# Performance work log

Hardware: AMD Instinct MI355X
Metric: run time of the kernel (lower is better)

## Reference

```python
import jax, jax.numpy as jnp
import numpy as np

B, C, N = 4, 256, 4096
BN_EPS = 1e-5


def setup_inputs() -> dict:
    key = jax.random.key(0)
    ks = jax.random.split(key, 8)
    Cq = C // 4
    return {
        "x": jax.random.normal(ks[0], (B, C, N), dtype=jnp.float32),
        # q_conv and k_conv share weights (self.q_conv.weight = self.k_conv.weight)
        "w_qk": jax.random.normal(ks[1], (Cq, C), dtype=jnp.float32) * 0.05,
        "w_v": jax.random.normal(ks[2], (C, C), dtype=jnp.float32) * 0.05,
        "b_v": jax.random.normal(ks[3], (C,), dtype=jnp.float32) * 0.05,
        # LBR: Conv1d(C,C,1) + BN1d (inference stats) + ReLU
        "w_lbr": jax.random.normal(ks[4], (C, C), dtype=jnp.float32) * 0.05,
        "b_lbr": jax.random.normal(ks[5], (C,), dtype=jnp.float32) * 0.05,
        "bn_gamma": jnp.ones((C,), dtype=jnp.float32),
        "bn_beta": jnp.zeros((C,), dtype=jnp.float32),
        "bn_mean": jax.random.normal(ks[6], (C,), dtype=jnp.float32) * 0.05,
        "bn_var": jax.random.uniform(ks[7], (C,), dtype=jnp.float32, minval=0.5, maxval=1.5),
    }


def reference(x, w_qk, w_v, b_v, w_lbr, b_lbr, bn_gamma, bn_beta, bn_mean, bn_var):
    # x: [B, C, N]
    chans = x.shape[1]
    # conv1x1 Q/K (shared weight, no bias), V (with bias)
    x_q = jnp.einsum('qc,bcn->bnq', w_qk, x)          # [B, N, C/4]
    x_k = jnp.einsum('qc,bcm->bqm', w_qk, x)          # [B, C/4, N]
    x_v = jnp.einsum('oc,bcn->bon', w_v, x) + b_v[None, :, None]  # [B, C, N]
    # energy: [B, N_query, N_key]
    energy = jnp.einsum('bnq,bqm->bnm', x_q, x_k)
    # 'SL' normalization: scale by C**-0.5, softmax over dim=-2 (query axis)
    energy = energy * (chans ** -0.5)
    attention = jax.nn.softmax(energy, axis=-2)        # [B, N, N]
    # x_r[b,c,m] = sum_n x_v[b,c,n] * attention[b,n,m]
    x_r = jnp.einsum('bcn,bnm->bcm', x_v, attention)   # [B, C, N]
    # offset residual
    x_r = x - x_r
    # LBR: conv1x1 -> BN (inference) -> ReLU
    h = jnp.einsum('oc,bcn->bon', w_lbr, x_r) + b_lbr[None, :, None]
    inv_std = jax.lax.rsqrt(bn_var + BN_EPS)
    h = (h - bn_mean[None, :, None]) * (inv_std * bn_gamma)[None, :, None] + bn_beta[None, :, None]
    h = jax.nn.relu(h)
    return x + h
```

## Files before the change

kernel.cpp:

```cpp
#include <hip/hip_runtime.h>
#include <hip/hip_bf16.h>
#include <stdint.h>
#include <math.h>

#define Bq 4
#define Cc 256
#define Nn 4096
#define CQ 64
#define QKSCALE 0.30028060219661246f

typedef short s16x4 __attribute__((ext_vector_type(4)));
typedef short s16x8 __attribute__((ext_vector_type(8)));
typedef unsigned int u32x4 __attribute__((ext_vector_type(4)));
typedef float f32x16 __attribute__((ext_vector_type(16)));

#define MFMA32(a,b,c) __builtin_amdgcn_mfma_f32_32x32x16_bf16((a),(b),(c),0,0,0)

static __device__ __forceinline__ unsigned short f2b(float f) {
  unsigned int u = __float_as_uint(f);
  u += 0x7FFFu + ((u >> 16) & 1u);
  return (unsigned short)(u >> 16);
}

static __device__ __forceinline__ unsigned short f2bh(float f) {
  __hip_bfloat16 h = __float2bfloat16(f);
  return __builtin_bit_cast(unsigned short, h);
}

static __device__ __forceinline__ float b2f(unsigned short u) {
  return __uint_as_float(((unsigned int)u) << 16);
}

static __device__ __forceinline__ float fexp2(float x) {
#if __has_builtin(__builtin_amdgcn_exp2f)
  return __builtin_amdgcn_exp2f(x);
#else
  return exp2f(x);
#endif
}

static __device__ __forceinline__ f32x16 fz16() {
  f32x16 z;
#pragma unroll
  for (int i = 0; i < 16; i++) z[i] = 0.0f;
  return z;
}

static __device__ __forceinline__ float sum16(f32x16 E) {
  return (((E[0] + E[1]) + (E[2] + E[3])) + ((E[4] + E[5]) + (E[6] + E[7]))) +
         (((E[8] + E[9]) + (E[10] + E[11])) + ((E[12] + E[13]) + (E[14] + E[15])));
}

__global__ __launch_bounds__(256) void k_prep(
    const float* __restrict__ wqk, const float* __restrict__ wv,
    const float* __restrict__ wlbr, const float* __restrict__ blbr,
    const float* __restrict__ gamma, const float* __restrict__ beta,
    const float* __restrict__ mean, const float* __restrict__ var,
    unsigned short* __restrict__ Wcat, float* __restrict__ sd) {
  int bx = blockIdx.x, t = threadIdx.x;
  if (bx < 576) {
    float v;
    if (bx < 64) v = wqk[bx * 256 + t] * QKSCALE;
    else if (bx < 320) v = wv[(bx - 64) * 256 + t];
    else v = wlbr[(bx - 320) * 256 + t];
    Wcat[bx * 256 + t] = f2b(v);
  } else {
    float s = gamma[t] * rsqrtf(var[t] + 1e-5f);
    sd[t] = s;
    sd[256 + t] = beta[t] + (blbr[t] - mean[t]) * s;
  }
}

__global__ __launch_bounds__(640) void k_proj(const float* __restrict__ x,
                                              const unsigned short* __restrict__ Wcat,
                                              const float* __restrict__ bv,
                                              unsigned short* __restrict__ qkT,
                                              unsigned short* __restrict__ Vf,
                                              unsigned short* __restrict__ xT) {
  __shared__ unsigned short xs[32 * 264];
  int bx = blockIdx.x;
  int b = bx >> 7;
  int ntile = bx & 127;
  int n0 = ntile * 32;
  int t = threadIdx.x;
  const float* xb = x + (size_t)b * Cc * Nn;
  for (int u = t; u < 1024; u += 640) {
    int c = u >> 2, j = (u & 3) * 8;
    const float* src = &xb[(size_t)c * Nn + n0 + j];
    float4 v0 = *(const float4*)src;
    float4 v1 = *(const float4*)(src + 4);
    xs[(j + 0) * 264 + c] = f2b(v0.x);
    xs[(j + 1) * 264 + c] = f2b(v0.y);
    xs[(j + 2) * 264 + c] = f2b(v0.z);
    xs[(j + 3) * 264 + c] = f2b(v0.w);
    xs[(j + 4) * 264 + c] = f2b(v1.x);
    xs[(j + 5) * 264 + c] = f2b(v1.y);
    xs[(j + 6) * 264 + c] = f2b(v1.z);
    xs[(j + 7) * 264 + c] = f2b(v1.w);
  }
  int w = t >> 6, a = t & 31, g = (t >> 5) & 1;
  bool isqk = (w >= 8);
  int row0 = isqk ? (w - 8) * 32 : 64 + w * 32;
  s16x8 wf[16];
#pragma unroll
  for (int kc = 0; kc < 16; kc++)
    wf[kc] = *(const s16x8*)&Wcat[(size_t)(row0 + a) * 256 + kc * 16 + 8 * g];
  __syncthreads();
  unsigned short* xTb = xT + ((size_t)b * Nn + n0) * Cc;
  for (int u = t; u < 1024; u += 640) {
    int row = u >> 5, ch = u & 31;
    *(s16x8*)&xTb[(size_t)row * Cc + ch * 8] = *(const s16x8*)&xs[row * 264 + ch * 8];
  }
  f32x16 acc = fz16();
#pragma unroll
  for (int kc = 0; kc < 16; kc++) {
    s16x8 xf = *(const s16x8*)&xs[a * 264 + kc * 16 + 8 * g];
    acc = MFMA32(xf, wf[kc], acc);
  }
  if (isqk) {
    unsigned short* dst = qkT + ((size_t)b * Nn + n0) * CQ;
    int q0 = row0;
#pragma unroll
    for (int r = 0; r < 16; r++) {
      int n = (r & 3) + 8 * (r >> 2) + 4 * g;
      dst[(size_t)n * CQ + q0 + a] = f2b(acc[r]);
    }
  } else {
    int c0 = row0 - 64;
    float bvv = bv[c0 + a];
    s16x8 vlo, vhi;
#pragma unroll
    for (int r = 0; r < 8; r++) {
      vlo[r] = (short)f2b(acc[r] + bvv);
      vhi[r] = (short)f2b(acc[8 + r] + bvv);
    }
    unsigned short* dstF =
        Vf + ((size_t)(b * 128 + ntile) * 4 + g) * 2048 + (size_t)(c0 + a) * 8;
    *(s16x8*)dstF = vlo;
    *(s16x8*)(dstF + 4096) = vhi;
  }
}

__global__ __launch_bounds__(256) void k_norm(const unsigned short* __restrict__ qkT,
                                              float* __restrict__ nrm) {
  int idx = blockIdx.x * 256 + threadIdx.x;
  const unsigned short* row = qkT + (size_t)idx * CQ;
  float s = 0.0f;
#pragma unroll
  for (int k = 0; k < 8; k++) {
    s16x8 v = *(const s16x8*)&row[k * 8];
#pragma unroll
    for (int j = 0; j < 8; j++) {
      float f = b2f((unsigned short)v[j]);
      s += f * f;
    }
  }
  nrm[idx] = sqrtf(s);
}

__global__ __launch_bounds__(512, 2) void k_attn(const unsigned short* __restrict__ qkT,
                                                 const unsigned short* __restrict__ Vf,
                                                 const float* __restrict__ nrm,
                                                 const unsigned short* __restrict__ Wcat,
                                                 const float* __restrict__ sd,
                                                 const unsigned short* __restrict__ xT,
                                                 const float* __restrict__ x,
                                                 float* __restrict__ out) {
  __shared__ __align__(16) float Pf[4 * 128 * 33];
  __shared__ float Ls[4 * 64];
  __shared__ unsigned short xs2[64 * 266];
  __shared__ float sdL[512];
  __shared__ float wmx[8];
  int bx = blockIdx.x;
  int id = ((bx & 7) << 5) | (bx >> 3);
  int b = id >> 6;
  int m0 = (id & 63) * 64;
  int t = threadIdx.x;
  int w = t >> 6, a = t & 31, g = (t >> 5) & 1;
  int cs = w >> 2, ns = w & 3;
  const unsigned short* qkTb = qkT + (size_t)b * Nn * CQ;
  sdL[t < 512 ? t : 0] = sd[t < 512 ? t : 0];
  const float* nrmb = nrm + (size_t)b * Nn;
  float lm = 0.0f;
#pragma unroll
  for (int i = 0; i < 8; i++) lm = fmaxf(lm, nrmb[t + i * 512]);
#pragma unroll
  for (int off = 1; off < 64; off <<= 1) lm = fmaxf(lm, __shfl_xor(lm, off, 64));
  if ((t & 63) == 0) wmx[w] = lm;
  __syncthreads();
  float mxf = fmaxf(fmaxf(fmaxf(wmx[0], wmx[1]), fmaxf(wmx[2], wmx[3])),
                    fmaxf(fmaxf(wmx[4], wmx[5]), fmaxf(wmx[6], wmx[7])));
  s16x8 Bq0[4], Bq1[4];
#pragma unroll
  for (int kc = 0; kc < 4; kc++) {
    Bq0[kc] = *(const s16x8*)&qkTb[(size_t)(m0 + a) * CQ + kc * 16 + 8 * g];
    Bq1[kc] = *(const s16x8*)&qkTb[(size_t)(m0 + 32 + a) * CQ + kc * 16 + 8 * g];
  }
  float Mh0 = nrmb[m0 + a] * mxf + 0.01f;
  float Mh1 = nrmb[m0 + 32 + a] * mxf + 0.01f;
  const unsigned short* Vc = Vf + (size_t)b * 1048576 + (size_t)g * 2048 +
                             (size_t)(cs * 128 + a) * 8;
  f32x16 acc[8];
#pragma unroll
  for (int i = 0; i < 8; i++) acc[i] = fz16();
  float Lp0 = 0.0f, Lp1 = 0.0f;
  s16x8 qf[4];
#pragma unroll
  for (int kc = 0; kc < 4; kc++)
    qf[kc] = *(const s16x8*)&qkTb[(size_t)(ns * 32 + a) * CQ + kc * 16 + 8 * g];
#pragma unroll 1
  for (int nt = ns; nt < 128; nt += 4) {
    const unsigned short* Vt = Vc + (size_t)nt * 8192;
    f32x16 E0 = fz16(), E1 = fz16();
#pragma unroll
    for (int kc = 0; kc < 4; kc++) E0 = MFMA32(qf[kc], Bq0[kc], E0);
    s16x8 va0, va1, va2, va3;
    va0 = *(const s16x8*)&Vt[0];
    va1 = *(const s16x8*)&Vt[4096];
    va2 = *(const s16x8*)&Vt[256];
    va3 = *(const s16x8*)&Vt[4096 + 256];
#pragma unroll
    for (int kc = 0; kc < 4; kc++) E1 = MFMA32(qf[kc], Bq1[kc], E1);
    int ntn = (nt + 4) & 127;
#pragma unroll
    for (int kc = 0; kc < 4; kc++)
      qf[kc] = *(const s16x8*)&qkTb[(size_t)(ntn * 32 + a) * CQ + kc * 16 + 8 * g];
#pragma unroll
    for (int r = 0; r < 16; r++) E0[r] = fexp2(E0[r] - Mh0);
    Lp0 += sum16(E0);
    s16x8 p00, p01;
#pragma unroll
    for (int j = 0; j < 8; j++) {
      p00[j] = (short)f2bh(E0[j]);
      p01[j] = (short)f2bh(E0[8 + j]);
    }
#pragma unroll
    for (int r = 0; r < 16; r++) E1[r] = fexp2(E1[r] - Mh1);
    Lp1 += sum16(E1);
    s16x8 p10, p11;
#pragma unroll
    for (int j = 0; j < 8; j++) {
      p10[j] = (short)f2bh(E1[j]);
      p11[j] = (short)f2bh(E1[8 + j]);
    }
    acc[0] = MFMA32(p00, va0, acc[0]);
    acc[4] = MFMA32(p10, va0, acc[4]);
    acc[1] = MFMA32(p00, va2, acc[1]);
    acc[5] = MFMA32(p10, va2, acc[5]);
    acc[0] = MFMA32(p01, va1, acc[0]);
    acc[4] = MFMA32(p11, va1, acc[4]);
    acc[1] = MFMA32(p01, va3, acc[1]);
    acc[5] = MFMA32(p11, va3, acc[5]);
    s16x8 vb0, vb1, vb2, vb3;
    vb0 = *(const s16x8*)&Vt[512];
    vb1 = *(const s16x8*)&Vt[4096 + 512];
    vb2 = *(const s16x8*)&Vt[768];
    vb3 = *(const s16x8*)&Vt[4096 + 768];
    acc[2] = MFMA32(p00, vb0, acc[2]);
    acc[6] = MFMA32(p10, vb0, acc[6]);
    acc[3] = MFMA32(p00, vb2, acc[3]);
    acc[7] = MFMA32(p10, vb2, acc[7]);
    acc[2] = MFMA32(p01, vb1, acc[2]);
    acc[6] = MFMA32(p11, vb1, acc[6]);
    acc[3] = MFMA32(p01, vb3, acc[3]);
    acc[7] = MFMA32(p11, vb3, acc[7]);
  }
  float Lw0 = Lp0 + __shfl_xor(Lp0, 32, 64);
  float Lw1 = Lp1 + __shfl_xor(Lp1, 32, 64);
  if (cs == 0 && (t & 63) < 32) {
    Ls[ns * 64 + a] = Lw0;
    Ls[ns * 64 + 32 + a] = Lw1;
  }
  const unsigned short* xTb = xT + ((size_t)b * Nn + m0) * Cc;
#pragma unroll
  for (int q = 0; q < 4; q++) {
    int qmt = q >> 1, qcs = q & 1;
    __syncthreads();
    if (cs == qcs) {
#pragma unroll
      for (int ct = 0; ct < 4; ct++) {
        float* dst = &Pf[(size_t)(ns * 128 + ct * 32 + a) * 33];
        f32x16 A = acc[qmt * 4 + ct];
#pragma unroll
        for (int r = 0; r < 16; r++) {
          int mrow = (r & 3) + 8 * (r >> 2) + 4 * g;
          dst[mrow] = A[r];
        }
      }
    }
    __syncthreads();
    int m = t & 31, c8 = t >> 5;
    float rL = 1.0f / (((Ls[qmt * 32 + m] + Ls[64 + qmt * 32 + m]) +
                        (Ls[128 + qmt * 32 + m] + Ls[192 + qmt * 32 + m])));
    const unsigned short* xrow = &xTb[(size_t)(qmt * 32 + m) * Cc + qcs * 128 + c8 * 8];
    s16x8 xv = *(const s16x8*)xrow;
#pragma unroll
    for (int j = 0; j < 8; j++) {
      int cl = c8 * 8 + j;
      float s = ((Pf[(0 * 128 + cl) * 33 + m] + Pf[(1 * 128 + cl) * 33 + m]) +
                 (Pf[(2 * 128 + cl) * 33 + m] + Pf[(3 * 128 + cl) * 33 + m]));
      xv[j] = (short)f2b(b2f((unsigned short)xv[j]) - s * rL);
    }
    *(s16x8*)&xs2[(size_t)(qmt * 32 + m) * 266 + qcs * 128 + c8 * 8] = xv;
  }
  __syncthreads();
  int o0 = w * 32;
  s16x8 wf[16];
#pragma unroll
  for (int kc = 0; kc < 16; kc++)
    wf[kc] = *(const s16x8*)&Wcat[(size_t)(320 + o0 + a) * 256 + kc * 16 + 8 * g];
  const float* xb = x + (size_t)b * Cc * Nn;
  float* ob = out + (size_t)b * Cc * Nn;
#pragma unroll
  for (int nsub = 0; nsub < 2; nsub++) {
    f32x16 ac2 = fz16();
#pragma unroll
    for (int kc = 0; kc < 16; kc++) {
      s16x8 xf = *(const s16x8*)&xs2[(size_t)(nsub * 32 + a) * 266 + kc * 16 + 8 * g];
      ac2 = MFMA32(wf[kc], xf, ac2);
    }
    int n = m0 + nsub * 32 + a;
#pragma unroll
    for (int r = 0; r < 16; r++) {
      int o = o0 + (r & 3) + 8 * (r >> 2) + 4 * g;
      float v = ac2[r] * sdL[o] + sdL[256 + o];
      v = fmaxf(v, 0.0f);
      ob[(size_t)o * Nn + n] = xb[(size_t)o * Nn + n] + v;
    }
  }
}

extern "C" void kernel_launch(void* const* d_in, const int* in_sizes, int n_in,
                              void* d_out, int out_size, void* d_ws, size_t ws_size,
                              hipStream_t stream) {
  (void)in_sizes; (void)n_in; (void)out_size; (void)ws_size;
  const float* x = (const float*)d_in[0];
  const float* wqk = (const float*)d_in[1];
  const float* wv = (const float*)d_in[2];
  const float* bv = (const float*)d_in[3];
  const float* wlbr = (const float*)d_in[4];
  const float* blbr = (const float*)d_in[5];
  const float* gamma = (const float*)d_in[6];
  const float* beta = (const float*)d_in[7];
  const float* mean = (const float*)d_in[8];
  const float* var = (const float*)d_in[9];
  char* ws = (char*)d_ws;
  unsigned short* qkT = (unsigned short*)ws;
  unsigned short* Vf = (unsigned short*)(ws + 2097152);
  unsigned short* xT = (unsigned short*)(ws + 10485760);
  float* sd = (float*)(ws + 18874368);
  unsigned short* Wcat = (unsigned short*)(ws + 18876416);
  float* nrm = (float*)(ws + 18876416 + 64 * 512);
  float* out = (float*)d_out;

  k_prep<<<dim3(577), dim3(256), 0, stream>>>(wqk, wv, wlbr, blbr, gamma, beta,
                                              mean, var, Wcat, sd);
  k_proj<<<dim3(512), dim3(640), 0, stream>>>(x, Wcat, bv, qkT, Vf, xT);
  k_norm<<<dim3(64), dim3(256), 0, stream>>>(qkT, nrm);
  k_attn<<<dim3(256), dim3(512), 0, stream>>>(qkT, Vf, nrm, Wcat, sd, xT, x, out);
}
```

Before: 95.75 us.

## Fuse row-norm into projection and drop transposed bf16 x copy

```diff
diff --git a/kernel.cpp b/kernel.cpp
--- a/kernel.cpp
+++ b/kernel.cpp
@@ -76,8 +76,9 @@
                                               const float* __restrict__ bv,
                                               unsigned short* __restrict__ qkT,
                                               unsigned short* __restrict__ Vf,
-                                              unsigned short* __restrict__ xT) {
+                                              float* __restrict__ nrm) {
   __shared__ unsigned short xs[32 * 264];
+  __shared__ float npart[64];
   int bx = blockIdx.x;
   int b = bx >> 7;
   int ntile = bx & 127;
@@ -106,11 +107,6 @@
   for (int kc = 0; kc < 16; kc++)
     wf[kc] = *(const s16x8*)&Wcat[(size_t)(row0 + a) * 256 + kc * 16 + 8 * g];
   __syncthreads();
-  unsigned short* xTb = xT + ((size_t)b * Nn + n0) * Cc;
-  for (int u = t; u < 1024; u += 640) {
-    int row = u >> 5, ch = u & 31;
-    *(s16x8*)&xTb[(size_t)row * Cc + ch * 8] = *(const s16x8*)&xs[row * 264 + ch * 8];
-  }
   f32x16 acc = fz16();
 #pragma unroll
   for (int kc = 0; kc < 16; kc++) {
@@ -124,6 +120,21 @@
     for (int r = 0; r < 16; r++) {
       int n = (r & 3) + 8 * (r >> 2) + 4 * g;
       dst[(size_t)n * CQ + q0 + a] = f2b(acc[r]);
+    }
+    float s2[16];
+#pragma unroll
+    for (int r = 0; r < 16; r++) {
+      float v = acc[r] * acc[r];
+#pragma unroll
+      for (int off = 1; off < 32; off <<= 1) v += __shfl_xor(v, off, 64);
+      s2[r] = v;
+    }
+    if ((t & 31) == 0) {
+#pragma unroll
+      for (int r = 0; r < 16; r++) {
+        int n = (r & 3) + 8 * (r >> 2) + 4 * g;
+        npart[(w - 8) * 32 + n] = s2[r];
+      }
     }
   } else {
     int c0 = row0 - 64;
@@ -139,23 +150,8 @@
     *(s16x8*)dstF = vlo;
     *(s16x8*)(dstF + 4096) = vhi;
   }
-}
-
-__global__ __launch_bounds__(256) void k_norm(const unsigned short* __restrict__ qkT,
-                                              float* __restrict__ nrm) {
-  int idx = blockIdx.x * 256 + threadIdx.x;
-  const unsigned short* row = qkT + (size_t)idx * CQ;
-  float s = 0.0f;
-#pragma unroll
-  for (int k = 0; k < 8; k++) {
-    s16x8 v = *(const s16x8*)&row[k * 8];
-#pragma unroll
-    for (int j = 0; j < 8; j++) {
-      float f = b2f((unsigned short)v[j]);
-      s += f * f;
-    }
-  }
-  nrm[idx] = sqrtf(s);
+  __syncthreads();
+  if (t < 32) nrm[(size_t)b * Nn + n0 + t] = sqrtf(npart[t] + npart[32 + t]);
 }
 
 __global__ __launch_bounds__(512, 2) void k_attn(const unsigned short* __restrict__ qkT,
@@ -163,7 +159,6 @@
                                                  const float* __restrict__ nrm,
                                                  const unsigned short* __restrict__ Wcat,
                                                  const float* __restrict__ sd,
-                                                 const unsigned short* __restrict__ xT,
                                                  const float* __restrict__ x,
                                                  float* __restrict__ out) {
   __shared__ __align__(16) float Pf[4 * 128 * 33];
@@ -271,10 +266,16 @@
     Ls[ns * 64 + a] = Lw0;
     Ls[ns * 64 + 32 + a] = Lw1;
   }
-  const unsigned short* xTb = xT + ((size_t)b * Nn + m0) * Cc;
+  const float* xb = x + (size_t)b * Cc * Nn;
+  float* ob = out + (size_t)b * Cc * Nn;
 #pragma unroll
   for (int q = 0; q < 4; q++) {
     int qmt = q >> 1, qcs = q & 1;
+    int m = t & 31, c8 = t >> 5;
+    float xq[8];
+#pragma unroll
+    for (int j = 0; j < 8; j++)
+      xq[j] = xb[(size_t)(qcs * 128 + c8 * 8 + j) * Nn + m0 + qmt * 32 + m];
     __syncthreads();
     if (cs == qcs) {
 #pragma unroll
@@ -289,17 +290,15 @@
       }
     }
     __syncthreads();
-    int m = t & 31, c8 = t >> 5;
     float rL = 1.0f / (((Ls[qmt * 32 + m] + Ls[64 + qmt * 32 + m]) +
                         (Ls[128 + qmt * 32 + m] + Ls[192 + qmt * 32 + m])));
-    const unsigned short* xrow = &xTb[(size_t)(qmt * 32 + m) * Cc + qcs * 128 + c8 * 8];
-    s16x8 xv = *(const s16x8*)xrow;
+    s16x8 xv;
 #pragma unroll
     for (int j = 0; j < 8; j++) {
-      int cl = c8 * 8 + j;
+      int cl = qcs * 128 + c8 * 8 + j;
       float s = ((Pf[(0 * 128 + cl) * 33 + m] + Pf[(1 * 128 + cl) * 33 + m]) +
                  (Pf[(2 * 128 + cl) * 33 + m] + Pf[(3 * 128 + cl) * 33 + m]));
-      xv[j] = (short)f2b(b2f((unsigned short)xv[j]) - s * rL);
+      xv[j] = (short)f2b(xq[j] - s * rL);
     }
     *(s16x8*)&xs2[(size_t)(qmt * 32 + m) * 266 + qcs * 128 + c8 * 8] = xv;
   }
@@ -309,8 +308,6 @@
 #pragma unroll
   for (int kc = 0; kc < 16; kc++)
     wf[kc] = *(const s16x8*)&Wcat[(size_t)(320 + o0 + a) * 256 + kc * 16 + 8 * g];
-  const float* xb = x + (size_t)b * Cc * Nn;
-  float* ob = out + (size_t)b * Cc * Nn;
 #pragma unroll
   for (int nsub = 0; nsub < 2; nsub++) {
     f32x16 ac2 = fz16();
@@ -347,15 +344,13 @@
   char* ws = (char*)d_ws;
   unsigned short* qkT = (unsigned short*)ws;
   unsigned short* Vf = (unsigned short*)(ws + 2097152);
-  unsigned short* xT = (unsigned short*)(ws + 10485760);
+  float* nrm = (float*)(ws + 10485760);
   float* sd = (float*)(ws + 18874368);
   unsigned short* Wcat = (unsigned short*)(ws + 18876416);
-  float* nrm = (float*)(ws + 18876416 + 64 * 512);
   float* out = (float*)d_out;
 
   k_prep<<<dim3(577), dim3(256), 0, stream>>>(wqk, wv, wlbr, blbr, gamma, beta,
                                               mean, var, Wcat, sd);
-  k_proj<<<dim3(512), dim3(640), 0, stream>>>(x, Wcat, bv, qkT, Vf, xT);
-  k_norm<<<dim3(64), dim3(256), 0, stream>>>(qkT, nrm);
-  k_attn<<<dim3(256), dim3(512), 0, stream>>>(qkT, Vf, nrm, Wcat, sd, xT, x, out);
-}
+  k_proj<<<dim3(512), dim3(640), 0, stream>>>(x, Wcat, bv, qkT, Vf, nrm);
+  k_attn<<<dim3(256), dim3(512), 0, stream>>>(qkT, Vf, nrm, Wcat, sd, x, out);
+}
```

After: 92.78 us, median of 2. 3.1% less time.
